# Performance work log

Measured on AMD Instinct MI355X. Metric: run time of the kernel, lower is better.

Reference implementation:

```python
import jax, jax.numpy as jnp
import numpy as np

N_NODES = 100000


def _gcn_layer(x, edge_index, W, b):
    # x: [N, Fin], edge_index: [2, E]
    row, col = edge_index[0], edge_index[1]
    n = x.shape[0]
    ones = jnp.ones(row.shape[0], dtype=x.dtype)
    deg = jax.ops.segment_sum(ones, row, num_segments=n)  # bincount(row)
    deg_inv_sqrt = jnp.where(deg > 0, deg ** -0.5, 0.0).astype(x.dtype)
    norm = deg_inv_sqrt[row] * deg_inv_sqrt[col]  # [E]
    h = x @ W + b  # linear first, as in the torch code
    # sparse COO matmul == scatter-add of norm-scaled source features into row
    msgs = norm[:, None] * h[col]  # [E, Fout]
    return jax.ops.segment_sum(msgs, row, num_segments=n)


def setup_inputs() -> dict:
    key = jax.random.key(0)
    ks = jax.random.split(key, 7)
    N, Fin, H, Fout = N_NODES, 256, 64, 64
    Epos, Eneg = 1600000, 1600000
    x = jax.random.normal(ks[0], (N, Fin), dtype=jnp.float32)
    pos_edge_index = jax.random.randint(ks[1], (2, Epos), 0, N, dtype=jnp.int64)
    neg_edge_index = jax.random.randint(ks[2], (2, Eneg), 0, N, dtype=jnp.int64)
    W1 = jax.random.normal(ks[3], (Fin, H), dtype=jnp.float32) * (1.0 / np.sqrt(Fin))
    b1 = jax.random.normal(ks[4], (H,), dtype=jnp.float32) * 0.01
    W2 = jax.random.normal(ks[5], (H, Fout), dtype=jnp.float32) * (1.0 / np.sqrt(H))
    b2 = jax.random.normal(ks[6], (Fout,), dtype=jnp.float32) * 0.01
    return {"x": x, "pos_edge_index": pos_edge_index, "neg_edge_index": neg_edge_index,
            "W1": W1, "b1": b1, "W2": W2, "b2": b2}


def reference(x, pos_edge_index, neg_edge_index, W1, b1, W2, b2):
    # encode: two GCN layers over pos_edge_index.
    # Note: the original calls self.PairNorm(x) but discards the result,
    # so PairNorm has no effect on the output.
    h = jax.nn.relu(_gcn_layer(x, pos_edge_index, W1, b1))
    z = _gcn_layer(h, pos_edge_index, W2, b2)  # [N, 64]
    # decode: dot product over concatenated pos+neg edges
    edge = jnp.concatenate([pos_edge_index, neg_edge_index], axis=-1)  # [2, Ep+En]
    return jnp.sum(z[edge[0]] * z[edge[1]], axis=-1)  # [Ep+En]
```

## Files before the change

### kernel.cpp

```cpp
#include <hip/hip_runtime.h>
#include <hip/hip_fp16.h>

#define FIN 256
#define FH  64
#define SCAN_BLK 1024
#define NCHUNK 8


__global__ __launch_bounds__(256) void deg_kernel(const int* __restrict__ rows,
                                                  unsigned* __restrict__ deg, int E) {
    int e = blockIdx.x * 256 + threadIdx.x;
    if (e < E) atomicAdd(&deg[rows[e]], 1u);
}


__global__ __launch_bounds__(256) void scan_block_kernel(const unsigned* __restrict__ deg,
                                                         int* __restrict__ rowptr,
                                                         int* __restrict__ blocksums, int N) {
    __shared__ int wsum[4];
    const int t = threadIdx.x;
    const int base = blockIdx.x * SCAN_BLK + t * 4;
    int d0 = 0, d1 = 0, d2 = 0, d3 = 0;
    if (base + 0 < N) d0 = (int)deg[base + 0];
    if (base + 1 < N) d1 = (int)deg[base + 1];
    if (base + 2 < N) d2 = (int)deg[base + 2];
    if (base + 3 < N) d3 = (int)deg[base + 3];
    const int tot = d0 + d1 + d2 + d3;
    const int lane = t & 63, wv = t >> 6;
    int inc = tot;
#pragma unroll
    for (int off = 1; off < 64; off <<= 1) {
        int v = __shfl_up(inc, off, 64);
        if (lane >= off) inc += v;
    }
    if (lane == 63) wsum[wv] = inc;
    __syncthreads();
    int woff = 0;
    for (int w = 0; w < wv; ++w) woff += wsum[w];
    const int ex = woff + inc - tot;
    if (base + 0 < N) rowptr[base + 0] = ex;
    if (base + 1 < N) rowptr[base + 1] = ex + d0;
    if (base + 2 < N) rowptr[base + 2] = ex + d0 + d1;
    if (base + 3 < N) rowptr[base + 3] = ex + d0 + d1 + d2;
    if (t == 255) blocksums[blockIdx.x] = woff + inc;
}


__global__ __launch_bounds__(256) void scan_add_kernel(int* __restrict__ rowptr,
                                                       int* __restrict__ cursor,
                                                       const unsigned* __restrict__ deg,
                                                       float* __restrict__ dis,
                                                       const int* __restrict__ blocksums,
                                                       int nb, int N, int E) {
    __shared__ int pre;
    const int t = threadIdx.x;
    const int i0 = blockIdx.x * 256;
    const int c0 = i0 / SCAN_BLK;
    if (t == 0) {
        int s = 0;
        for (int k = 0; k < c0; ++k) s += blocksums[k];
        pre = s;
    }
    __syncthreads();
    int i = i0 + t;
    if (i < N) {
        int v = rowptr[i] + pre;
        rowptr[i] = v;
        cursor[i] = v;
        unsigned d = deg[i];
        dis[i] = d ? 1.0f / sqrtf((float)d) : 0.0f;
    }
    if (i == 0) rowptr[N] = E;
}


__global__ __launch_bounds__(256) void scatter_edges_kernel(const int* __restrict__ rows,
                                                            const int* __restrict__ cols,
                                                            int* __restrict__ cursor,
                                                            int* __restrict__ colOut,
                                                            int* __restrict__ einv,
                                                            float chunk_scale, int E) {
    const int chunk = blockIdx.x & (NCHUNK - 1);
    const int eb = blockIdx.x >> 3;
    int e = eb * 256 + threadIdx.x;
    if (e >= E) return;
    int r = rows[e];
    int rc = (int)((float)r * chunk_scale);
    rc = rc > (NCHUNK - 1) ? (NCHUNK - 1) : rc;
    if (rc == chunk) {
        int p = atomicAdd(&cursor[r], 1);
        colOut[p] = cols[e];
        einv[p] = e;
    }
}


__global__ __launch_bounds__(256) void gemm1_kernel(const float* __restrict__ x,
                                                    const float* __restrict__ W,
                                                    const float* __restrict__ b,
                                                    const float* __restrict__ dis,
                                                    __half2* __restrict__ outh, int N) {
    __shared__ float xs[32][132];
    __shared__ float ws[32][64];
    const int t = threadIdx.x;
    const int rb = blockIdx.x * 128;
    const int rg = t >> 3, cg = t & 7;
    const int r0 = rg * 4, c0 = cg * 8;
    float acc[4][8];
#pragma unroll
    for (int i = 0; i < 4; ++i)
#pragma unroll
        for (int j = 0; j < 8; ++j) acc[i][j] = 0.f;

    const float4* x4 = (const float4*)x;
    const int kk = (t & 7) * 4;
    const int rloc = t >> 3;

    for (int k0 = 0; k0 < FIN; k0 += 32) {
        __syncthreads();
        {
            const float4* w4 = (const float4*)(W + k0 * 64);
            float4* wl = (float4*)&ws[0][0];
            wl[t]       = w4[t];
            wl[t + 256] = w4[t + 256];
        }
#pragma unroll
        for (int p = 0; p < 4; ++p) {
            int r = rloc + p * 32;
            int gr = rb + r; if (gr >= N) gr = N - 1;
            float4 v = x4[gr * 64 + (k0 >> 2) + (t & 7)];
            xs[kk + 0][r] = v.x; xs[kk + 1][r] = v.y;
            xs[kk + 2][r] = v.z; xs[kk + 3][r] = v.w;
        }
        __syncthreads();
#pragma unroll
        for (int k = 0; k < 32; ++k) {
            float4 xa = *(const float4*)&xs[k][r0];
            float4 wa = *(const float4*)&ws[k][c0];
            float4 wb = *(const float4*)&ws[k][c0 + 4];
            float xr[4] = {xa.x, xa.y, xa.z, xa.w};
            float wr[8] = {wa.x, wa.y, wa.z, wa.w, wb.x, wb.y, wb.z, wb.w};
#pragma unroll
            for (int i = 0; i < 4; ++i)
#pragma unroll
                for (int j = 0; j < 8; ++j) acc[i][j] = fmaf(xr[i], wr[j], acc[i][j]);
        }
    }
    float bias[8];
#pragma unroll
    for (int j = 0; j < 8; ++j) bias[j] = b[c0 + j];
#pragma unroll
    for (int i = 0; i < 4; ++i) {
        int gr = rb + r0 + i;
        if (gr < N) {
            float d = dis[gr];
            __half2 o[4];
            o[0] = __floats2half2_rn((acc[i][0] + bias[0]) * d, (acc[i][1] + bias[1]) * d);
            o[1] = __floats2half2_rn((acc[i][2] + bias[2]) * d, (acc[i][3] + bias[3]) * d);
            o[2] = __floats2half2_rn((acc[i][4] + bias[4]) * d, (acc[i][5] + bias[5]) * d);
            o[3] = __floats2half2_rn((acc[i][6] + bias[6]) * d, (acc[i][7] + bias[7]) * d);
            *(uint4*)&outh[gr * 32 + (c0 >> 1)] = *(uint4*)o;
        }
    }
}


__global__ __launch_bounds__(256) void gather_agg16_kernel(const int* __restrict__ rowptr,
                                                           const int* __restrict__ cols,
                                                           const __half2* __restrict__ h2v,
                                                           const float* __restrict__ dscale,
                                                           float* __restrict__ outf,
                                                           __half2* __restrict__ outh,
                                                           int N, int tohalf) {
    int r = blockIdx.x * 8 + (threadIdx.x >> 5);
    int l32 = threadIdx.x & 31;
    if (r >= N) return;
    const int rowbase = threadIdx.x & 32;
    int s = rowptr[r], e = rowptr[r + 1];
    float2 acc[8];
#pragma unroll
    for (int u = 0; u < 8; ++u) { acc[u].x = 0.f; acc[u].y = 0.f; }
    for (int base = s; base < e; base += 32) {
        int n = e - base; if (n > 32) n = 32;
        int idx = (l32 < n) ? cols[base + l32] : 0;
        int j = 0;
        for (; j + 15 < n; j += 16) {
            __half2 tv[16];
#pragma unroll
            for (int u = 0; u < 16; ++u) {
                int c = __shfl(idx, rowbase + j + u);
                tv[u] = h2v[(size_t)c * 32 + l32];
            }
#pragma unroll
            for (int u = 0; u < 16; ++u) {
                float2 f = __half22float2(tv[u]);
                acc[u & 7].x += f.x; acc[u & 7].y += f.y;
            }
        }
        for (; j + 3 < n; j += 4) {
            __half2 tv[4];
#pragma unroll
            for (int u = 0; u < 4; ++u) {
                int c = __shfl(idx, rowbase + j + u);
                tv[u] = h2v[(size_t)c * 32 + l32];
            }
#pragma unroll
            for (int u = 0; u < 4; ++u) {
                float2 f = __half22float2(tv[u]);
                acc[u].x += f.x; acc[u].y += f.y;
            }
        }
        for (; j < n; ++j) {
            int c = __shfl(idx, rowbase + j);
            float2 f = __half22float2(h2v[(size_t)c * 32 + l32]);
            acc[0].x += f.x; acc[0].y += f.y;
        }
    }
    float2 v;
    v.x = ((acc[0].x + acc[1].x) + (acc[2].x + acc[3].x)) + ((acc[4].x + acc[5].x) + (acc[6].x + acc[7].x));
    v.y = ((acc[0].y + acc[1].y) + (acc[2].y + acc[3].y)) + ((acc[4].y + acc[5].y) + (acc[6].y + acc[7].y));
    if (dscale) { float d = dscale[r]; v.x *= d; v.y *= d; }
    if (tohalf) outh[(size_t)r * 32 + l32] = __float22half2_rn(v);
    else        *(float2*)&outf[(size_t)r * 64 + l32 * 2] = v;
}


__global__ __launch_bounds__(256) void gemm2_kernel(const float* __restrict__ agg,
                                                    const float* __restrict__ dis,
                                                    const float* __restrict__ W,
                                                    const float* __restrict__ b,
                                                    __half2* __restrict__ outh, int N) {
    __shared__ float xs[64][132];
    __shared__ float ws[64][64];
    const int t = threadIdx.x;
    const int rb = blockIdx.x * 128;
    {
        const float4* w4 = (const float4*)W;
        float4* wl = (float4*)&ws[0][0];
#pragma unroll
        for (int p = 0; p < 4; ++p) wl[p * 256 + t] = w4[p * 256 + t];
    }
    {
        const float4* a4 = (const float4*)agg;
        const int c4 = (t & 15) * 4;
        const int rloc = t >> 4;
#pragma unroll
        for (int p = 0; p < 8; ++p) {
            int r = rloc + p * 16;
            int gr = rb + r; if (gr >= N) gr = N - 1;
            float d = dis[gr];
            float4 v = a4[gr * 16 + (t & 15)];
            xs[c4 + 0][r] = fmaxf(v.x * d, 0.f);
            xs[c4 + 1][r] = fmaxf(v.y * d, 0.f);
            xs[c4 + 2][r] = fmaxf(v.z * d, 0.f);
            xs[c4 + 3][r] = fmaxf(v.w * d, 0.f);
        }
    }
    __syncthreads();
    const int rg = t >> 3, cg = t & 7;
    const int r0 = rg * 4, c0 = cg * 8;
    float acc[4][8];
#pragma unroll
    for (int i = 0; i < 4; ++i)
#pragma unroll
        for (int j = 0; j < 8; ++j) acc[i][j] = 0.f;
#pragma unroll 16
    for (int k = 0; k < 64; ++k) {
        float4 xa = *(const float4*)&xs[k][r0];
        float4 wa = *(const float4*)&ws[k][c0];
        float4 wb = *(const float4*)&ws[k][c0 + 4];
        float xr[4] = {xa.x, xa.y, xa.z, xa.w};
        float wr[8] = {wa.x, wa.y, wa.z, wa.w, wb.x, wb.y, wb.z, wb.w};
#pragma unroll
        for (int i = 0; i < 4; ++i)
#pragma unroll
            for (int j = 0; j < 8; ++j) acc[i][j] = fmaf(xr[i], wr[j], acc[i][j]);
    }
    float bias[8];
#pragma unroll
    for (int j = 0; j < 8; ++j) bias[j] = b[c0 + j];
#pragma unroll
    for (int i = 0; i < 4; ++i) {
        int gr = rb + r0 + i;
        if (gr < N) {
            float d = dis[gr];
            __half2 o[4];
            o[0] = __floats2half2_rn((acc[i][0] + bias[0]) * d, (acc[i][1] + bias[1]) * d);
            o[1] = __floats2half2_rn((acc[i][2] + bias[2]) * d, (acc[i][3] + bias[3]) * d);
            o[2] = __floats2half2_rn((acc[i][4] + bias[4]) * d, (acc[i][5] + bias[5]) * d);
            o[3] = __floats2half2_rn((acc[i][6] + bias[6]) * d, (acc[i][7] + bias[7]) * d);
            *(uint4*)&outh[gr * 32 + (c0 >> 1)] = *(uint4*)o;
        }
    }
}


__device__ __forceinline__ float dot8h(float4 A, float4 B) {
    union { float4 f; __half2 h[4]; } ua, ub;
    ua.f = A; ub.f = B;
    float s = 0.f;
#pragma unroll
    for (int k = 0; k < 4; ++k) {
        float2 fa = __half22float2(ua.h[k]);
        float2 fb = __half22float2(ub.h[k]);
        s = fmaf(fa.x, fb.x, s);
        s = fmaf(fa.y, fb.y, s);
    }
    return s;
}

__global__ __launch_bounds__(256) void decode16_kernel(const int* __restrict__ rowptr,
                                                       const int* __restrict__ cols,
                                                       const int* __restrict__ einv,
                                                       const int* __restrict__ ne,
                                                       const float4* __restrict__ zf4,
                                                       float* __restrict__ outp,
                                                       int N, int negB, int Ep, int En) {
    const int t = threadIdx.x;
    const int l8 = t & 7;

    if ((int)blockIdx.x < negB) {
        const int g = t >> 3;
        const int base = blockIdx.x * 256;
        int a[8], b[8];
        bool v[8];
#pragma unroll
        for (int q = 0; q < 8; ++q) {
            int e = base + q * 32 + g;
            v[q] = e < En;
            a[q] = 0; b[q] = 0;
            if (v[q]) { a[q] = ne[e]; b[q] = ne[En + e]; }
        }
        float4 va[8], vb[8];
#pragma unroll
        for (int q = 0; q < 8; ++q) {
            va[q] = zf4[(size_t)a[q] * 8 + l8];
            vb[q] = zf4[(size_t)b[q] * 8 + l8];
        }
#pragma unroll
        for (int q = 0; q < 8; ++q) {
            float p = dot8h(va[q], vb[q]);
            p += __shfl_xor(p, 4);
            p += __shfl_xor(p, 2);
            p += __shfl_xor(p, 1);
            int e = base + q * 32 + g;
            if (v[q] && l8 == 0) outp[Ep + e] = p;
        }
    } else {
        int r = (blockIdx.x - negB) * 8 + (t >> 5);
        if (r >= N) return;
        const int l32 = t & 31;
        const int rowbase = t & 32;
        const int g4 = (t >> 3) & 3;
        int s = rowptr[r], e = rowptr[r + 1];
        if (s == e) return;
        float zr8[8];
        {
            union { float4 f; __half2 h[4]; } uz;
            uz.f = zf4[(size_t)r * 8 + l8];
#pragma unroll
            for (int k = 0; k < 4; ++k) {
                float2 f = __half22float2(uz.h[k]);
                zr8[2 * k] = f.x; zr8[2 * k + 1] = f.y;
            }
        }
        for (int base = s; base < e; base += 32) {
            int n = e - base; if (n > 32) n = 32;
            int idx = (l32 < n) ? cols[base + l32] : 0;
            int ei  = (l32 < n) ? einv[base + l32] : 0;
            for (int j = 0; j < n; j += 8) {
                int pos0 = j + g4, pos1 = j + 4 + g4;
                bool a0 = pos0 < n, a1 = pos1 < n;
                int c0 = __shfl(idx, rowbase + (a0 ? pos0 : 0));
                int c1 = __shfl(idx, rowbase + (a1 ? pos1 : 0));
                int d0 = __shfl(ei, rowbase + (a0 ? pos0 : 0));
                int d1 = __shfl(ei, rowbase + (a1 ? pos1 : 0));
                float4 v0 = zf4[(size_t)c0 * 8 + l8];
                float4 v1 = zf4[(size_t)c1 * 8 + l8];
                union { float4 f; __half2 h[4]; } u0, u1;
                u0.f = v0; u1.f = v1;
                float p0 = 0.f, p1 = 0.f;
#pragma unroll
                for (int k = 0; k < 4; ++k) {
                    float2 f0 = __half22float2(u0.h[k]);
                    float2 f1 = __half22float2(u1.h[k]);
                    p0 = fmaf(zr8[2 * k], f0.x, p0); p0 = fmaf(zr8[2 * k + 1], f0.y, p0);
                    p1 = fmaf(zr8[2 * k], f1.x, p1); p1 = fmaf(zr8[2 * k + 1], f1.y, p1);
                }
                p0 += __shfl_xor(p0, 4); p0 += __shfl_xor(p0, 2); p0 += __shfl_xor(p0, 1);
                p1 += __shfl_xor(p1, 4); p1 += __shfl_xor(p1, 2); p1 += __shfl_xor(p1, 1);
                if (l8 == 0) {
                    if (a0) outp[d0] = p0;
                    if (a1) outp[d1] = p1;
                }
            }
        }
    }
}


extern "C" void kernel_launch(void* const* d_in, const int* in_sizes, int n_in,
                              void* d_out, int out_size, void* d_ws, size_t ws_size,
                              hipStream_t stream) {
    const float* x  = (const float*)d_in[0];
    const int*   pe = (const int*)d_in[1];
    const int*   ne = (const int*)d_in[2];
    const float* W1 = (const float*)d_in[3];
    const float* b1 = (const float*)d_in[4];
    const float* W2 = (const float*)d_in[5];
    const float* b2 = (const float*)d_in[6];
    float* outp = (float*)d_out;

    const int N  = in_sizes[0] / FIN;
    const int Ep = in_sizes[1] / 2;
    const int En = in_sizes[2] / 2;

    char* w = (char*)d_ws;
    size_t off = 0;
    auto alloc = [&](size_t bytes) {
        void* p = w + off;
        off = (off + bytes + 255) & ~(size_t)255;
        return p;
    };
    unsigned* deg   = (unsigned*)alloc((size_t)N * 4);
    float* dis      = (float*)alloc((size_t)N * 4);
    int* rowptr     = (int*)alloc((size_t)(N + 1) * 4);
    int* cursor     = (int*)alloc((size_t)N * 4);
    int* blocksums  = (int*)alloc(((size_t)N / SCAN_BLK + 2) * 4);
    int* colsorted  = (int*)alloc((size_t)Ep * 4);
    int* einv       = (int*)alloc((size_t)Ep * 4);
    __half2* A16    = (__half2*)alloc((size_t)N * 64 * 2);
    float* B        = (float*)alloc((size_t)N * 64 * 4);

    const int nscan = (N + SCAN_BLK - 1) / SCAN_BLK;
    const int nEdgeBlocks = (Ep + 255) / 256;

    hipMemsetAsync(deg, 0, (size_t)N * 4, stream);

    deg_kernel<<<nEdgeBlocks, 256, 0, stream>>>(pe, deg, Ep);
    scan_block_kernel<<<nscan, 256, 0, stream>>>(deg, rowptr, blocksums, N);
    scan_add_kernel<<<(N + 255) / 256, 256, 0, stream>>>(rowptr, cursor, deg, dis,
                                                         blocksums, nscan, N, Ep);
    scatter_edges_kernel<<<nEdgeBlocks * NCHUNK, 256, 0, stream>>>(
        pe, pe + Ep, cursor, colsorted, einv, (float)NCHUNK / (float)N, Ep);
    gemm1_kernel<<<(N + 127) / 128, 256, 0, stream>>>(x, W1, b1, dis, A16, N);
    gather_agg16_kernel<<<(N + 7) / 8, 256, 0, stream>>>(rowptr, colsorted, A16, nullptr,
                                                         B, nullptr, N, 0);
    gemm2_kernel<<<(N + 127) / 128, 256, 0, stream>>>(B, dis, W2, b2, A16, N);
    __half2* z16 = (__half2*)B;
    gather_agg16_kernel<<<(N + 7) / 8, 256, 0, stream>>>(rowptr, colsorted, A16, dis,
                                                         nullptr, z16, N, 1);
    const int negB = (En + 255) / 256;
    const int posB = (N + 7) / 8;
    decode16_kernel<<<negB + posB, 256, 0, stream>>>(rowptr, colsorted, einv, ne,
                                                     (const float4*)z16, outp,
                                                     N, negB, Ep, En);
}
```

Before: 521.2 us.

## Write positive-edge scores in CSR order, then permute with a separate gather kernel

The decode kernel now writes positive-edge dot products to a contiguous CSR-ordered buffer, reusing the A16 buffer. It no longer loads einv and scatters to random output positions. A new permute kernel gathers these into edge order using an inverse index that the scatter pass now writes as inv[e]=p. Several streaming loads and stores (x in gemm1, agg in gemm2, aggregation output, negative-edge output) are also marked nontemporal to reduce cache pollution. The cost is an extra kernel launch and an extra pass over Ep floats, in exchange for coalesced writes in decode.

New measurement: 531.3 us. No clear change (+1.9%).

```diff
diff --git a/kernel.cpp b/kernel.cpp
--- a/kernel.cpp
+++ b/kernel.cpp
@@ -5,6 +5,9 @@
 #define FH  64
 #define SCAN_BLK 1024
 #define NCHUNK 8
+
+typedef float f4v __attribute__((ext_vector_type(4)));
+typedef float f2v __attribute__((ext_vector_type(2)));
 
 
 __global__ __launch_bounds__(256) void deg_kernel(const int* __restrict__ rows,
@@ -78,7 +81,7 @@
                                                             const int* __restrict__ cols,
                                                             int* __restrict__ cursor,
                                                             int* __restrict__ colOut,
-                                                            int* __restrict__ einv,
+                                                            int* __restrict__ inv,
                                                             float chunk_scale, int E) {
     const int chunk = blockIdx.x & (NCHUNK - 1);
     const int eb = blockIdx.x >> 3;
@@ -90,7 +93,7 @@
     if (rc == chunk) {
         int p = atomicAdd(&cursor[r], 1);
         colOut[p] = cols[e];
-        einv[p] = e;
+        inv[e] = p;
     }
 }
 
@@ -112,7 +115,7 @@
 #pragma unroll
         for (int j = 0; j < 8; ++j) acc[i][j] = 0.f;
 
-    const float4* x4 = (const float4*)x;
+    const f4v* x4 = (const f4v*)x;
     const int kk = (t & 7) * 4;
     const int rloc = t >> 3;
 
@@ -128,7 +131,7 @@
         for (int p = 0; p < 4; ++p) {
             int r = rloc + p * 32;
             int gr = rb + r; if (gr >= N) gr = N - 1;
-            float4 v = x4[gr * 64 + (k0 >> 2) + (t & 7)];
+            f4v v = __builtin_nontemporal_load(&x4[gr * 64 + (k0 >> 2) + (t & 7)]);
             xs[kk + 0][r] = v.x; xs[kk + 1][r] = v.y;
             xs[kk + 2][r] = v.z; xs[kk + 3][r] = v.w;
         }
@@ -220,8 +223,12 @@
     v.x = ((acc[0].x + acc[1].x) + (acc[2].x + acc[3].x)) + ((acc[4].x + acc[5].x) + (acc[6].x + acc[7].x));
     v.y = ((acc[0].y + acc[1].y) + (acc[2].y + acc[3].y)) + ((acc[4].y + acc[5].y) + (acc[6].y + acc[7].y));
     if (dscale) { float d = dscale[r]; v.x *= d; v.y *= d; }
-    if (tohalf) outh[(size_t)r * 32 + l32] = __float22half2_rn(v);
-    else        *(float2*)&outf[(size_t)r * 64 + l32 * 2] = v;
+    if (tohalf) {
+        outh[(size_t)r * 32 + l32] = __float22half2_rn(v);
+    } else {
+        f2v o; o.x = v.x; o.y = v.y;
+        __builtin_nontemporal_store(o, (f2v*)&outf[(size_t)r * 64 + l32 * 2]);
+    }
 }
 
 
@@ -241,7 +248,7 @@
         for (int p = 0; p < 4; ++p) wl[p * 256 + t] = w4[p * 256 + t];
     }
     {
-        const float4* a4 = (const float4*)agg;
+        const f4v* a4 = (const f4v*)agg;
         const int c4 = (t & 15) * 4;
         const int rloc = t >> 4;
 #pragma unroll
@@ -249,7 +256,7 @@
             int r = rloc + p * 16;
             int gr = rb + r; if (gr >= N) gr = N - 1;
             float d = dis[gr];
-            float4 v = a4[gr * 16 + (t & 15)];
+            f4v v = __builtin_nontemporal_load(&a4[gr * 16 + (t & 15)]);
             xs[c4 + 0][r] = fmaxf(v.x * d, 0.f);
             xs[c4 + 1][r] = fmaxf(v.y * d, 0.f);
             xs[c4 + 2][r] = fmaxf(v.z * d, 0.f);
@@ -311,9 +318,9 @@
 
 __global__ __launch_bounds__(256) void decode16_kernel(const int* __restrict__ rowptr,
                                                        const int* __restrict__ cols,
-                                                       const int* __restrict__ einv,
                                                        const int* __restrict__ ne,
                                                        const float4* __restrict__ zf4,
+                                                       float* __restrict__ P,
                                                        float* __restrict__ outp,
                                                        int N, int negB, int Ep, int En) {
     const int t = threadIdx.x;
@@ -344,7 +351,7 @@
             p += __shfl_xor(p, 2);
             p += __shfl_xor(p, 1);
             int e = base + q * 32 + g;
-            if (v[q] && l8 == 0) outp[Ep + e] = p;
+            if (v[q] && l8 == 0) __builtin_nontemporal_store(p, &outp[Ep + e]);
         }
     } else {
         int r = (blockIdx.x - negB) * 8 + (t >> 5);
@@ -367,14 +374,11 @@
         for (int base = s; base < e; base += 32) {
             int n = e - base; if (n > 32) n = 32;
             int idx = (l32 < n) ? cols[base + l32] : 0;
-            int ei  = (l32 < n) ? einv[base + l32] : 0;
             for (int j = 0; j < n; j += 8) {
                 int pos0 = j + g4, pos1 = j + 4 + g4;
                 bool a0 = pos0 < n, a1 = pos1 < n;
                 int c0 = __shfl(idx, rowbase + (a0 ? pos0 : 0));
                 int c1 = __shfl(idx, rowbase + (a1 ? pos1 : 0));
-                int d0 = __shfl(ei, rowbase + (a0 ? pos0 : 0));
-                int d1 = __shfl(ei, rowbase + (a1 ? pos1 : 0));
                 float4 v0 = zf4[(size_t)c0 * 8 + l8];
                 float4 v1 = zf4[(size_t)c1 * 8 + l8];
                 union { float4 f; __half2 h[4]; } u0, u1;
@@ -390,11 +394,22 @@
                 p0 += __shfl_xor(p0, 4); p0 += __shfl_xor(p0, 2); p0 += __shfl_xor(p0, 1);
                 p1 += __shfl_xor(p1, 4); p1 += __shfl_xor(p1, 2); p1 += __shfl_xor(p1, 1);
                 if (l8 == 0) {
-                    if (a0) outp[d0] = p0;
-                    if (a1) outp[d1] = p1;
+                    if (a0) P[base + pos0] = p0;
+                    if (a1) P[base + pos1] = p1;
                 }
             }
         }
+    }
+}
+
+
+__global__ __launch_bounds__(256) void permute_kernel(const float* __restrict__ P,
+                                                      const int* __restrict__ inv,
+                                                      float* __restrict__ out, int E) {
+    int e = blockIdx.x * 256 + threadIdx.x;
+    if (e < E) {
+        int p = __builtin_nontemporal_load(&inv[e]);
+        __builtin_nontemporal_store(P[p], &out[e]);
     }
 }
 
@@ -428,7 +443,7 @@
     int* cursor     = (int*)alloc((size_t)N * 4);
     int* blocksums  = (int*)alloc(((size_t)N / SCAN_BLK + 2) * 4);
     int* colsorted  = (int*)alloc((size_t)Ep * 4);
-    int* einv       = (int*)alloc((size_t)Ep * 4);
+    int* inv        = (int*)alloc((size_t)Ep * 4);
     __half2* A16    = (__half2*)alloc((size_t)N * 64 * 2);
     float* B        = (float*)alloc((size_t)N * 64 * 4);
 
@@ -442,7 +457,7 @@
     scan_add_kernel<<<(N + 255) / 256, 256, 0, stream>>>(rowptr, cursor, deg, dis,
                                                          blocksums, nscan, N, Ep);
     scatter_edges_kernel<<<nEdgeBlocks * NCHUNK, 256, 0, stream>>>(
-        pe, pe + Ep, cursor, colsorted, einv, (float)NCHUNK / (float)N, Ep);
+        pe, pe + Ep, cursor, colsorted, inv, (float)NCHUNK / (float)N, Ep);
     gemm1_kernel<<<(N + 127) / 128, 256, 0, stream>>>(x, W1, b1, dis, A16, N);
     gather_agg16_kernel<<<(N + 7) / 8, 256, 0, stream>>>(rowptr, colsorted, A16, nullptr,
                                                          B, nullptr, N, 0);
@@ -450,9 +465,11 @@
     __half2* z16 = (__half2*)B;
     gather_agg16_kernel<<<(N + 7) / 8, 256, 0, stream>>>(rowptr, colsorted, A16, dis,
                                                          nullptr, z16, N, 1);
+    float* P = (float*)A16;
     const int negB = (En + 255) / 256;
     const int posB = (N + 7) / 8;
-    decode16_kernel<<<negB + posB, 256, 0, stream>>>(rowptr, colsorted, einv, ne,
-                                                     (const float4*)z16, outp,
+    decode16_kernel<<<negB + posB, 256, 0, stream>>>(rowptr, colsorted, ne,
+                                                     (const float4*)z16, P, outp,
                                                      N, negB, Ep, En);
-}
+    permute_kernel<<<(Ep + 255) / 256, 256, 0, stream>>>(P, inv, outp, Ep);
+}
```
